# Optimization experiments

Hardware: AMD Instinct MI355X
Metric: run time of the kernel (lower is better)

Reference implementation:

```python
import jax, jax.numpy as jnp
import numpy as np

N_NODES = 20000
N_EDGES = 8192
UNITS = 128
NUM_GAUSSIANS = 50
CUTOFF = 8.0
GAMMA = 10.0
MIN_DIST, MAX_DIST = 0.0, 30.0


def setup_inputs() -> dict:
    key = jax.random.key(0)
    ks = jax.random.split(key, 6)
    node_features = jax.random.normal(ks[0], (N_NODES, UNITS), dtype=jnp.float32)
    edge_indices = jax.random.randint(ks[1], (2, N_EDGES), 0, N_NODES, dtype=jnp.int32)
    distances = jax.random.uniform(ks[2], (N_EDGES,), dtype=jnp.float32)
    # filter network params (Dense(units) -> swish -> Dense(units*units))
    W1 = jax.random.normal(ks[3], (NUM_GAUSSIANS, UNITS), dtype=jnp.float32) / np.sqrt(NUM_GAUSSIANS)
    b1 = jnp.zeros((UNITS,), dtype=jnp.float32)
    W2 = jax.random.normal(ks[4], (UNITS, UNITS * UNITS), dtype=jnp.float32) / np.sqrt(UNITS)
    b2 = jnp.zeros((UNITS * UNITS,), dtype=jnp.float32)
    # transform Dense(units, use_bias=False)
    Wt = jax.random.normal(ks[5], (UNITS, UNITS), dtype=jnp.float32) / np.sqrt(UNITS)
    return {"node_features": node_features, "edge_indices": edge_indices,
            "distances": distances, "W1": W1, "b1": b1, "W2": W2, "b2": b2, "Wt": Wt}


def reference(node_features, edge_indices, distances, W1, b1, W2, b2, Wt):
    n_nodes, units = node_features.shape
    # cutoff mask (multiplicative; dropped edges contribute zero to the scatter-sum,
    # equivalent to tf.boolean_mask + unsorted_segment_sum)
    mask = (distances <= CUTOFF).astype(node_features.dtype)  # [E]
    # Gaussian basis expansion
    centers = jnp.linspace(MIN_DIST, MAX_DIST, NUM_GAUSSIANS, dtype=jnp.float32)
    df = jnp.exp(-GAMMA * jnp.square(distances[:, None] - centers[None, :]))  # [E, G]
    # filter network: Dense -> swish -> Dense(units*units)
    h = jax.nn.silu(df @ W1 + b1)                    # [E, U]
    filters = (h @ W2 + b2).reshape(-1, units, units)  # [E, U, U]
    # gather source node features, transform, per-edge matvec
    src = node_features[edge_indices[0]]             # [E, U]
    transformed = src @ Wt                           # [E, U]
    filtered = jnp.einsum('eij,ej->ei', filters, transformed) * mask[:, None]  # [E, U]
    # scatter-sum to destination nodes
    messages = jax.ops.segment_sum(filtered, edge_indices[1], num_segments=n_nodes)
    return jax.nn.silu(messages)
```

## Files before the change

### kernel.cpp

```cpp
#include <hip/hip_runtime.h>
#include <hip/hip_fp16.h>


typedef _Float16 f16;
typedef __attribute__((ext_vector_type(8))) f16 f16x8;
typedef __attribute__((ext_vector_type(4))) float f32x4;
typedef __attribute__((ext_vector_type(4))) unsigned int u32x4;

#define NEDGE 8192
#define NNODE 20000
#define NG    50
#define KSTEPS 516
#define W2C_BYTES (KSTEPS * 8192)
#define HT_BYTES (64 * 132 * 128 * 2)
#define TM_BYTES (NEDGE * 128 * 2)

#define LDS_H   0
#define LDS_TM  5120
#define LDS_TOT 37888

static __device__ __forceinline__ float fsilu(float x) { return x / (1.0f + __expf(-x)); }

static __device__ __forceinline__ void gll16(const void* g, void* l) {
  __builtin_amdgcn_global_load_lds(
      (const __attribute__((address_space(1))) unsigned int*)g,
      (__attribute__((address_space(3))) unsigned int*)l, 16, 0, 0);
}

__global__ __launch_bounds__(256) void k01(const float* __restrict__ W2,
                                           const float* __restrict__ b2,
                                           const float* __restrict__ NF,
                                           const int*   __restrict__ EI,
                                           const float* __restrict__ DI,
                                           const float* __restrict__ W1,
                                           const float* __restrict__ B1,
                                           const float* __restrict__ WT,
                                           f16* __restrict__ w2c,
                                           f16* __restrict__ ht2,
                                           f16* __restrict__ tmo,
                                           float* __restrict__ out, int nz4) {
  __shared__ float df[16][NG];
  __shared__ float s_mask[16];
  __shared__ float s_src[16][128];
  __shared__ float t_tile[16][132];
  __shared__ float h_tile[16][132];
  const int bid = blockIdx.x, tid = threadIdx.x;

  if (bid < 1032) {
    int gidx = bid * 256 + tid;
    int lane = gidx & 63;
    int nt   = (gidx >> 6) & 7;
    int step = gidx >> 9;
    int k0i = step * 32 + (lane >> 4) * 8;
    int i   = nt * 16 + (lane & 15);
    int u   = k0i >> 7, j0 = k0i & 127;
    const float* src = (u < 128) ? (W2 + (size_t)u * 16384 + i * 128 + j0)
                                 : (b2 + i * 128 + j0);
    union { f16 s[8]; u32x4 v; } pk;
#pragma unroll
    for (int r = 0; r < 8; ++r) pk.s[r] = (f16)src[r];
    *((u32x4*)w2c + gidx) = pk.v;
    return;
  }
  if (bid < 1544) {
    int et = bid - 1032, e0 = et * 16;
    for (int idx = tid; idx < 16 * NG; idx += 256) {
      int e = idx / NG, g = idx - e * NG;
      float d = DI[e0 + e];
      float x = d - (float)g * (30.0f / 49.0f);
      df[e][g] = __expf(-10.0f * x * x);
    }
    if (tid < 16) s_mask[tid] = (DI[e0 + tid] <= 8.0f) ? 1.0f : 0.0f;
    for (int idx = tid; idx < 16 * 128; idx += 256) {
      int e = idx >> 7, u = idx & 127;
      s_src[e][u] = NF[(size_t)EI[e0 + e] * 128 + u];
    }
    __syncthreads();

    int j = tid & 127, es = tid >> 7;
    for (int e = es * 8; e < es * 8 + 8; ++e) {
      float acc = B1[j];
      for (int g = 0; g < NG; ++g) acc += df[e][g] * W1[g * 128 + j];
      h_tile[e][j] = fsilu(acc);
    }
    {
      float acc[8] = {0.f,0.f,0.f,0.f,0.f,0.f,0.f,0.f};
      for (int u = 0; u < 128; ++u) {
        float wv = WT[u * 128 + j];
#pragma unroll
        for (int e8 = 0; e8 < 8; ++e8) acc[e8] += s_src[es * 8 + e8][u] * wv;
      }
#pragma unroll
      for (int e8 = 0; e8 < 8; ++e8) t_tile[es * 8 + e8][j] = acc[e8];
    }
    __syncthreads();

    int eb = et >> 3, el0 = (et & 7) * 16;
    {
      int u = tid >> 1, hf = tid & 1;
      union { f16 s[8]; u32x4 v; } pk;
#pragma unroll
      for (int k = 0; k < 8; ++k) pk.s[k] = (f16)h_tile[hf * 8 + k][u];
      *(u32x4*)(ht2 + ((size_t)eb * 132 + u) * 128 + el0 + hf * 8) = pk.v;
    }
    if (tid < 16) ht2[((size_t)eb * 132 + 128) * 128 + el0 + tid] = (f16)1.0f;
    {
      int e = tid >> 4, cc = tid & 15;
      float m = s_mask[e];
      union { f16 s[8]; u32x4 v; } pk;
#pragma unroll
      for (int k = 0; k < 8; ++k) pk.s[k] = (f16)(m * t_tile[e][cc * 8 + k]);
      int col = (cc * 16) ^ ((e & 7) << 4);
      *(u32x4*)((char*)tmo + (size_t)(e0 + e) * 256 + col) = pk.v;
    }
    return;
  }
  {
    int base = (bid - 1544) * 1024;
    f32x4 z = {0.f, 0.f, 0.f, 0.f};
#pragma unroll
    for (int k = 0; k < 4; ++k) {
      int i4 = base + k * 256 + tid;
      if (i4 < nz4) ((f32x4*)out)[i4] = z;
    }
  }
}

__global__ __launch_bounds__(256, 2) void k2_gemm(const f16* __restrict__ w2c,
                                                  const f16* __restrict__ ht2,
                                                  const f16* __restrict__ tm,
                                                  const int* __restrict__ EI,
                                                  float* __restrict__ msg) {
  __shared__ u32x4 smem_v[LDS_TOT / 16];
  char* smem = (char*)smem_v;

  const int bid = blockIdx.x;
  const int c   = bid & 7;
  const int eb  = bid >> 3;
  const int e0  = eb * 128;
  const int nu  = (c == 7) ? 17 : 16;
  const int tid = threadIdx.x, w = tid >> 6, lane = tid & 63;
  const int l15 = lane & 15, g4 = lane >> 4;
  const int wm = w >> 1, wn = w & 1;

  {
    const char* tsrc = (const char*)tm + (size_t)e0 * 256 + w * 8192;
#pragma unroll
    for (int q = 0; q < 8; ++q)
      gll16(tsrc + q * 1024 + lane * 16,
            smem + LDS_TM + w * 8192 + q * 1024 + lane * 16);
  }
  if (w == 0) {
    const char* hsrc = (const char*)ht2 + ((size_t)eb * 132 + c * 16) * 256;
#pragma unroll
    for (int q = 0; q < 5; ++q)
      gll16(hsrc + q * 1024 + lane * 16, smem + LDS_H + q * 1024 + lane * 16);
  }
  __syncthreads();

  f16x8 Tall[4][4];
  {
    const int tmrow = LDS_TM + (wm * 64 + l15) * 256;
    const int colsw = (l15 & 7) << 4;
#pragma unroll
    for (int rt = 0; rt < 4; ++rt)
#pragma unroll
      for (int jc = 0; jc < 4; ++jc)
        Tall[rt][jc] = *(const f16x8*)(smem + tmrow + rt * 4096 +
                                       ((jc * 64 + g4 * 16) ^ colsw));
  }
  const __half* hbase = (const __half*)(smem + LDS_H) + wm * 64 + l15;

  __half2 hc[4], hn[4];
#pragma unroll
  for (int rt = 0; rt < 4; ++rt) hc[rt] = __half2half2(hbase[rt * 16]);

  const char* bp = (const char*)w2c + (size_t)(c * 64) * 8192 + wn * 4096 + lane * 16;
  const size_t offmax = (size_t)(nu * 4 - 1) * 8192;
  f16x8 B0[4], B1[4];
#pragma unroll
  for (int nt = 0; nt < 4; ++nt) B0[nt] = *(const f16x8*)(bp + nt * 1024);
#pragma unroll
  for (int nt = 0; nt < 4; ++nt) B1[nt] = *(const f16x8*)(bp + 8192 + nt * 1024);
  size_t off = 2 * 8192;

  f32x4 acc[4][4];
#pragma unroll
  for (int rt = 0; rt < 4; ++rt)
#pragma unroll
    for (int nt = 0; nt < 4; ++nt) acc[rt][nt] = (f32x4){0.f, 0.f, 0.f, 0.f};

  for (int u = 0; u < nu; ++u) {
#pragma unroll
    for (int jc = 0; jc < 4; ++jc) {
      if (jc == 1) {
#pragma unroll
        for (int rt = 0; rt < 4; ++rt)
          hn[rt] = __half2half2(hbase[(u + 1) * 128 + rt * 16]);
      }
      union uf { f16x8 v; __half2 h[4]; };
      uf a[4];
#pragma unroll
      for (int rt = 0; rt < 4; ++rt) {
        uf t; t.v = Tall[rt][jc];
#pragma unroll
        for (int q = 0; q < 4; ++q) a[rt].h[q] = __hmul2(t.h[q], hc[rt]);
      }
      size_t o = off; if (o > offmax) o = offmax;
      __builtin_amdgcn_s_setprio(1);
#pragma unroll
      for (int nt = 0; nt < 4; ++nt) {
        if ((jc & 1) == 0) {
#pragma unroll
          for (int rt = 0; rt < 4; ++rt)
            acc[rt][nt] = __builtin_amdgcn_mfma_f32_16x16x32_f16(a[rt].v, B0[nt], acc[rt][nt], 0, 0, 0);
          B0[nt] = *(const f16x8*)(bp + o + nt * 1024);
        } else {
#pragma unroll
          for (int rt = 0; rt < 4; ++rt)
            acc[rt][nt] = __builtin_amdgcn_mfma_f32_16x16x32_f16(a[rt].v, B1[nt], acc[rt][nt], 0, 0, 0);
          B1[nt] = *(const f16x8*)(bp + o + nt * 1024);
        }
      }
      __builtin_amdgcn_s_setprio(0);
      off += 8192;
    }
#pragma unroll
    for (int rt = 0; rt < 4; ++rt) hc[rt] = hn[rt];
  }

  const int* dst = EI + NEDGE;
#pragma unroll
  for (int rt = 0; rt < 4; ++rt) {
#pragma unroll
    for (int r = 0; r < 4; ++r) {
      int e = e0 + wm * 64 + rt * 16 + g4 * 4 + r;
      float* row = msg + (size_t)dst[e] * 128 + wn * 64 + l15;
#pragma unroll
      for (int nt = 0; nt < 4; ++nt)
        atomicAdd(row + nt * 16, acc[rt][nt][r]);
    }
  }
}

__global__ __launch_bounds__(256) void k3_silu(float* __restrict__ out, int n4) {
  int idx = blockIdx.x * 256 + threadIdx.x;
  int stride = gridDim.x * 256;
  f32x4* p = (f32x4*)out;
  for (; idx < n4; idx += stride) {
    f32x4 v = p[idx];
#pragma unroll
    for (int cc = 0; cc < 4; ++cc) v[cc] = fsilu(v[cc]);
    p[idx] = v;
  }
}

extern "C" void kernel_launch(void* const* d_in, const int* in_sizes, int n_in,
                              void* d_out, int out_size, void* d_ws, size_t ws_size,
                              hipStream_t stream) {
  const float* NF = (const float*)d_in[0];
  const int*   EI = (const int*)  d_in[1];
  const float* DI = (const float*)d_in[2];
  const float* W1 = (const float*)d_in[3];
  const float* B1 = (const float*)d_in[4];
  const float* W2 = (const float*)d_in[5];
  const float* B2 = (const float*)d_in[6];
  const float* WT = (const float*)d_in[7];
  float* out = (float*)d_out;

  f16* w2c = (f16*)d_ws;
  f16* ht2 = (f16*)((char*)d_ws + W2C_BYTES);
  f16* tmo = (f16*)((char*)d_ws + W2C_BYTES + HT_BYTES);
  size_t needed = (size_t)W2C_BYTES + HT_BYTES + TM_BYTES;
  if (ws_size < needed) return;

  int nz4 = out_size / 4;
  int zb  = (nz4 + 1023) / 1024;
  k01    <<<dim3(1544 + zb), dim3(256), 0, stream>>>(W2, B2, NF, EI, DI, W1, B1, WT,
                                                     w2c, ht2, tmo, out, nz4);
  k2_gemm<<<dim3(512),       dim3(256), 0, stream>>>(w2c, ht2, tmo, EI, out);
  k3_silu<<<dim3(1024),      dim3(256), 0, stream>>>(out, out_size / 4);
}
```

Measured before the change: 88.42 us.

## Accumulate messages in fp16 via packed atomics and restage W2 conversion through LDS

The scatter-sum target moves from an fp32 output buffer to an fp16 workspace buffer. Neighbouring lanes are combined with a shuffle so each pair issues one packed fp16 atomic add, which halves the atomic count and the bytes touched. The W2 fp16 conversion now uses one block per row: it loads coalesced float4s into LDS and then writes MFMA-fragment order, replacing 1032 blocks of strided scalar loads. The final SiLU kernel reads fp16 and writes fp32. The prefetch offset clamp is removed, so the last iteration may prefetch past the active range. fp16 accumulation of sums risks precision loss and overflow.

```diff
diff --git a/kernel.cpp b/kernel.cpp
--- a/kernel.cpp
+++ b/kernel.cpp
@@ -14,6 +14,7 @@
 #define W2C_BYTES (KSTEPS * 8192)
 #define HT_BYTES (64 * 132 * 128 * 2)
 #define TM_BYTES (NEDGE * 128 * 2)
+#define MSGH_BYTES (NNODE * 128 * 2)
 
 #define LDS_H   0
 #define LDS_TM  5120
@@ -38,60 +39,68 @@
                                            f16* __restrict__ w2c,
                                            f16* __restrict__ ht2,
                                            f16* __restrict__ tmo,
-                                           float* __restrict__ out, int nz4) {
-  __shared__ float df[16][NG];
-  __shared__ float s_mask[16];
-  __shared__ float s_src[16][128];
-  __shared__ float t_tile[16][132];
-  __shared__ float h_tile[16][132];
+                                           __half* __restrict__ msgh) {
+  __shared__ union {
+    f16 row[16384];
+    struct {
+      float df[16][NG]; float mask[16]; float src[16][128];
+      float tt[16][132]; float ht[16][132];
+    } k1;
+  } sm;
   const int bid = blockIdx.x, tid = threadIdx.x;
 
-  if (bid < 1032) {
-    int gidx = bid * 256 + tid;
-    int lane = gidx & 63;
-    int nt   = (gidx >> 6) & 7;
-    int step = gidx >> 9;
-    int k0i = step * 32 + (lane >> 4) * 8;
-    int i   = nt * 16 + (lane & 15);
-    int u   = k0i >> 7, j0 = k0i & 127;
-    const float* src = (u < 128) ? (W2 + (size_t)u * 16384 + i * 128 + j0)
-                                 : (b2 + i * 128 + j0);
-    union { f16 s[8]; u32x4 v; } pk;
-#pragma unroll
-    for (int r = 0; r < 8; ++r) pk.s[r] = (f16)src[r];
-    *((u32x4*)w2c + gidx) = pk.v;
+  if (bid < 129) {
+    const int u = bid;
+    const float* src = (u < 128) ? (W2 + (size_t)u * 16384) : b2;
+#pragma unroll
+    for (int it = 0; it < 16; ++it) {
+      int idx = it * 1024 + tid * 4;
+      f32x4 v = *(const f32x4*)(src + idx);
+#pragma unroll
+      for (int r = 0; r < 4; ++r) sm.row[idx + r] = (f16)v[r];
+    }
+    __syncthreads();
+#pragma unroll
+    for (int q = 0; q < 8; ++q) {
+      int fi = q * 256 + tid;
+      int lane = fi & 63, nt = (fi >> 6) & 7, s = fi >> 9;
+      int i = nt * 16 + (lane & 15);
+      int j = s * 32 + (lane >> 4) * 8;
+      u32x4 frag = *(const u32x4*)&sm.row[i * 128 + j];
+      *((u32x4*)w2c + (size_t)(u * 4 + s) * 512 + nt * 64 + lane) = frag;
+    }
     return;
   }
-  if (bid < 1544) {
-    int et = bid - 1032, e0 = et * 16;
+  if (bid < 641) {
+    int et = bid - 129, e0 = et * 16;
     for (int idx = tid; idx < 16 * NG; idx += 256) {
       int e = idx / NG, g = idx - e * NG;
       float d = DI[e0 + e];
       float x = d - (float)g * (30.0f / 49.0f);
-      df[e][g] = __expf(-10.0f * x * x);
-    }
-    if (tid < 16) s_mask[tid] = (DI[e0 + tid] <= 8.0f) ? 1.0f : 0.0f;
+      sm.k1.df[e][g] = __expf(-10.0f * x * x);
+    }
+    if (tid < 16) sm.k1.mask[tid] = (DI[e0 + tid] <= 8.0f) ? 1.0f : 0.0f;
     for (int idx = tid; idx < 16 * 128; idx += 256) {
       int e = idx >> 7, u = idx & 127;
-      s_src[e][u] = NF[(size_t)EI[e0 + e] * 128 + u];
+      sm.k1.src[e][u] = NF[(size_t)EI[e0 + e] * 128 + u];
     }
     __syncthreads();
 
     int j = tid & 127, es = tid >> 7;
     for (int e = es * 8; e < es * 8 + 8; ++e) {
       float acc = B1[j];
-      for (int g = 0; g < NG; ++g) acc += df[e][g] * W1[g * 128 + j];
-      h_tile[e][j] = fsilu(acc);
+      for (int g = 0; g < NG; ++g) acc += sm.k1.df[e][g] * W1[g * 128 + j];
+      sm.k1.ht[e][j] = fsilu(acc);
     }
     {
       float acc[8] = {0.f,0.f,0.f,0.f,0.f,0.f,0.f,0.f};
       for (int u = 0; u < 128; ++u) {
         float wv = WT[u * 128 + j];
 #pragma unroll
-        for (int e8 = 0; e8 < 8; ++e8) acc[e8] += s_src[es * 8 + e8][u] * wv;
-      }
-#pragma unroll
-      for (int e8 = 0; e8 < 8; ++e8) t_tile[es * 8 + e8][j] = acc[e8];
+        for (int e8 = 0; e8 < 8; ++e8) acc[e8] += sm.k1.src[es * 8 + e8][u] * wv;
+      }
+#pragma unroll
+      for (int e8 = 0; e8 < 8; ++e8) sm.k1.tt[es * 8 + e8][j] = acc[e8];
     }
     __syncthreads();
 
@@ -100,28 +109,28 @@
       int u = tid >> 1, hf = tid & 1;
       union { f16 s[8]; u32x4 v; } pk;
 #pragma unroll
-      for (int k = 0; k < 8; ++k) pk.s[k] = (f16)h_tile[hf * 8 + k][u];
+      for (int k = 0; k < 8; ++k) pk.s[k] = (f16)sm.k1.ht[hf * 8 + k][u];
       *(u32x4*)(ht2 + ((size_t)eb * 132 + u) * 128 + el0 + hf * 8) = pk.v;
     }
     if (tid < 16) ht2[((size_t)eb * 132 + 128) * 128 + el0 + tid] = (f16)1.0f;
     {
       int e = tid >> 4, cc = tid & 15;
-      float m = s_mask[e];
+      float m = sm.k1.mask[e];
       union { f16 s[8]; u32x4 v; } pk;
 #pragma unroll
-      for (int k = 0; k < 8; ++k) pk.s[k] = (f16)(m * t_tile[e][cc * 8 + k]);
+      for (int k = 0; k < 8; ++k) pk.s[k] = (f16)(m * sm.k1.tt[e][cc * 8 + k]);
       int col = (cc * 16) ^ ((e & 7) << 4);
       *(u32x4*)((char*)tmo + (size_t)(e0 + e) * 256 + col) = pk.v;
     }
     return;
   }
   {
-    int base = (bid - 1544) * 1024;
-    f32x4 z = {0.f, 0.f, 0.f, 0.f};
+    int base = (bid - 641) * 1024;
+    u32x4 z = {0u, 0u, 0u, 0u};
 #pragma unroll
     for (int k = 0; k < 4; ++k) {
       int i4 = base + k * 256 + tid;
-      if (i4 < nz4) ((f32x4*)out)[i4] = z;
+      if (i4 < (MSGH_BYTES / 16)) ((u32x4*)msgh)[i4] = z;
     }
   }
 }
@@ -130,7 +139,7 @@
                                                   const f16* __restrict__ ht2,
                                                   const f16* __restrict__ tm,
                                                   const int* __restrict__ EI,
-                                                  float* __restrict__ msg) {
+                                                  __half* __restrict__ msgh) {
   __shared__ u32x4 smem_v[LDS_TOT / 16];
   char* smem = (char*)smem_v;
 
@@ -176,7 +185,6 @@
   for (int rt = 0; rt < 4; ++rt) hc[rt] = __half2half2(hbase[rt * 16]);
 
   const char* bp = (const char*)w2c + (size_t)(c * 64) * 8192 + wn * 4096 + lane * 16;
-  const size_t offmax = (size_t)(nu * 4 - 1) * 8192;
   f16x8 B0[4], B1[4];
 #pragma unroll
   for (int nt = 0; nt < 4; ++nt) B0[nt] = *(const f16x8*)(bp + nt * 1024);
@@ -206,7 +214,6 @@
 #pragma unroll
         for (int q = 0; q < 4; ++q) a[rt].h[q] = __hmul2(t.h[q], hc[rt]);
       }
-      size_t o = off; if (o > offmax) o = offmax;
       __builtin_amdgcn_s_setprio(1);
 #pragma unroll
       for (int nt = 0; nt < 4; ++nt) {
@@ -214,12 +221,12 @@
 #pragma unroll
           for (int rt = 0; rt < 4; ++rt)
             acc[rt][nt] = __builtin_amdgcn_mfma_f32_16x16x32_f16(a[rt].v, B0[nt], acc[rt][nt], 0, 0, 0);
-          B0[nt] = *(const f16x8*)(bp + o + nt * 1024);
+          B0[nt] = *(const f16x8*)(bp + off + nt * 1024);
         } else {
 #pragma unroll
           for (int rt = 0; rt < 4; ++rt)
             acc[rt][nt] = __builtin_amdgcn_mfma_f32_16x16x32_f16(a[rt].v, B1[nt], acc[rt][nt], 0, 0, 0);
-          B1[nt] = *(const f16x8*)(bp + o + nt * 1024);
+          B1[nt] = *(const f16x8*)(bp + off + nt * 1024);
         }
       }
       __builtin_amdgcn_s_setprio(0);
@@ -235,24 +242,40 @@
 #pragma unroll
     for (int r = 0; r < 4; ++r) {
       int e = e0 + wm * 64 + rt * 16 + g4 * 4 + r;
-      float* row = msg + (size_t)dst[e] * 128 + wn * 64 + l15;
-#pragma unroll
-      for (int nt = 0; nt < 4; ++nt)
-        atomicAdd(row + nt * 16, acc[rt][nt][r]);
-    }
-  }
-}
-
-__global__ __launch_bounds__(256) void k3_silu(float* __restrict__ out, int n4) {
+      size_t rowb = (size_t)dst[e] * 128 + wn * 64;
+#pragma unroll
+      for (int nt = 0; nt < 4; ++nt) {
+        float v  = acc[rt][nt][r];
+        float pv = __shfl_xor(v, 1, 64);
+        if ((l15 & 1) == 0) {
+          __half2 h2;
+          h2.x = __float2half_rn(v);
+          h2.y = __float2half_rn(pv);
+          unsigned int d = *(unsigned int*)&h2;
+          unsigned long long addr =
+              (unsigned long long)(msgh + rowb + nt * 16 + l15);
+          asm volatile("global_atomic_pk_add_f16 %0, %1, off"
+                       :: "v"(addr), "v"(d) : "memory");
+        }
+      }
+    }
+  }
+}
+
+__global__ __launch_bounds__(256) void k3_silu(const __half* __restrict__ msgh,
+                                               float* __restrict__ out, int n8) {
   int idx = blockIdx.x * 256 + threadIdx.x;
-  int stride = gridDim.x * 256;
-  f32x4* p = (f32x4*)out;
-  for (; idx < n4; idx += stride) {
-    f32x4 v = p[idx];
-#pragma unroll
-    for (int cc = 0; cc < 4; ++cc) v[cc] = fsilu(v[cc]);
-    p[idx] = v;
-  }
+  if (idx >= n8) return;
+  union { u32x4 v; __half h[8]; } r;
+  r.v = *(const u32x4*)(msgh + (size_t)idx * 8);
+  f32x4 o0, o1;
+#pragma unroll
+  for (int cc = 0; cc < 4; ++cc) {
+    o0[cc] = fsilu(__half2float(r.h[cc]));
+    o1[cc] = fsilu(__half2float(r.h[4 + cc]));
+  }
+  *(f32x4*)(out + (size_t)idx * 8)     = o0;
+  *(f32x4*)(out + (size_t)idx * 8 + 4) = o1;
 }
 
 extern "C" void kernel_launch(void* const* d_in, const int* in_sizes, int n_in,
@@ -268,16 +291,15 @@
   const float* WT = (const float*)d_in[7];
   float* out = (float*)d_out;
 
-  f16* w2c = (f16*)d_ws;
-  f16* ht2 = (f16*)((char*)d_ws + W2C_BYTES);
-  f16* tmo = (f16*)((char*)d_ws + W2C_BYTES + HT_BYTES);
-  size_t needed = (size_t)W2C_BYTES + HT_BYTES + TM_BYTES;
+  f16*    w2c  = (f16*)d_ws;
+  f16*    ht2  = (f16*)((char*)d_ws + W2C_BYTES);
+  f16*    tmo  = (f16*)((char*)d_ws + W2C_BYTES + HT_BYTES);
+  __half* msgh = (__half*)((char*)d_ws + W2C_BYTES + HT_BYTES + TM_BYTES);
+  size_t needed = (size_t)W2C_BYTES + HT_BYTES + TM_BYTES + MSGH_BYTES;
   if (ws_size < needed) return;
 
-  int nz4 = out_size / 4;
-  int zb  = (nz4 + 1023) / 1024;
-  k01    <<<dim3(1544 + zb), dim3(256), 0, stream>>>(W2, B2, NF, EI, DI, W1, B1, WT,
-                                                     w2c, ht2, tmo, out, nz4);
-  k2_gemm<<<dim3(512),       dim3(256), 0, stream>>>(w2c, ht2, tmo, EI, out);
-  k3_silu<<<dim3(1024),      dim3(256), 0, stream>>>(out, out_size / 4);
-}
+  k01    <<<dim3(954),  dim3(256), 0, stream>>>(W2, B2, NF, EI, DI, W1, B1, WT,
+                                                w2c, ht2, tmo, msgh);
+  k2_gemm<<<dim3(512),  dim3(256), 0, stream>>>(w2c, ht2, tmo, EI, msgh);
+  k3_silu<<<dim3(1250), dim3(256), 0, stream>>>(msgh, out, NNODE * 128 / 8);
+}
```

After: 94.66 us. 1.07x slower.
